# Kernel tuning notes

Measured on AMD Instinct MI355X. Metric: run time of the kernel, lower is better.

Reference implementation:

```python
import jax, jax.numpy as jnp
import numpy as np

N_ENT = 200000; N_USR = 100000; D = 64
E = 1500000; NI = 1000000
HOPS = 2; N_ITER = 3; N_VIRT = 3; N_REL = 11
EPS = 1e-12


def setup_inputs() -> dict:
    key = jax.random.key(0)
    ks = jax.random.split(key, 8)
    entity_emb = jax.random.normal(ks[0], (N_ENT, D), jnp.float32) * 0.1
    user_emb = jax.random.normal(ks[1], (N_USR, D), jnp.float32) * 0.1
    latent_emb = jax.random.normal(ks[2], (N_VIRT, D), jnp.float32)
    rel_weight = jax.random.normal(ks[3], (N_REL - 1, D), jnp.float32)
    # per-hop Aggregator.w, initialized as in the module
    agg_w = jnp.tile(jnp.array([0.4, 0.3, 0.3], jnp.float32), (HOPS, 1))
    edge_index = jax.random.randint(ks[4], (2, E), 0, N_ENT)
    edge_type = jax.random.randint(ks[5], (E,), 1, N_REL)  # values in [1, n_relations-1]
    user_index = jax.random.randint(ks[6], (NI,), 0, N_USR)
    item_index = jax.random.randint(ks[7], (NI,), 0, N_ENT)
    return dict(entity_emb=entity_emb, user_emb=user_emb, latent_emb=latent_emb,
                rel_weight=rel_weight, agg_w=agg_w, edge_index=edge_index,
                edge_type=edge_type, user_index=user_index, item_index=item_index)


def _l2norm(x):
    n = jnp.linalg.norm(x, axis=1, keepdims=True)
    return x / jnp.maximum(n, EPS)


def _squash(u):
    sq = jnp.sum(u * u, axis=1, keepdims=True)  # ||u||^2
    return (sq / (sq + 1.0)) * _l2norm(u)


def _lws_entity(entity_emb, head, tail, mask_f):
    """LWS over a single virtual-relation edge subset (mask_f zeroes other edges).
    Matches torch: neigh is cumulatively sim-scaled across iterations."""
    cnt = jax.ops.segment_sum(mask_f, head, num_segments=N_ENT)
    denom = jnp.maximum(cnt, 1.0)[:, None]
    neigh = entity_emb[tail] * mask_f[:, None]          # [E, D]
    u = None
    for it in range(N_ITER):
        if u is not None:
            sim = jnp.sum(u[head] * neigh, axis=1, keepdims=True)
            neigh = sim * neigh
        u = jax.ops.segment_sum(neigh, head, num_segments=N_ENT) / denom
        if it < N_ITER - 1:
            u = _squash(u)
        u = u + entity_emb
    return u


def _lws_user(entity_emb, user_emb, user_index, item_index):
    """LWS for users; neigh is re-gathered fresh each iteration (as in torch)."""
    ones = jnp.ones((item_index.shape[0],), entity_emb.dtype)
    cnt = jax.ops.segment_sum(ones, user_index, num_segments=N_USR)
    denom = jnp.maximum(cnt, 1.0)[:, None]
    u = None
    for it in range(N_ITER):
        neigh = entity_emb[item_index]                  # [NI, D]
        if u is not None:
            sim = jnp.sum(u[user_index] * neigh, axis=1, keepdims=True)
            neigh = sim * neigh
        u = jax.ops.segment_sum(neigh, user_index, num_segments=N_USR) / denom
        if it < N_ITER - 1:
            u = _squash(u)
        u = u + user_emb
    return u


def reference(entity_emb, user_emb, latent_emb, rel_weight, agg_w,
              edge_index, edge_type, user_index, item_index):
    head, tail = edge_index[0], edge_index[1]
    # relation -> virtual-relation routing (argmax over similarity)
    relation_remap = jnp.argmax(rel_weight @ latent_emb.T, axis=1)   # [n_rel-1]
    et = relation_remap[edge_type - 1]                               # [E] in [0, N_VIRT)

    entity_res = entity_emb
    user_res = user_emb
    ent = entity_emb
    usr = user_emb
    for hop in range(HOPS):
        items = [_lws_entity(ent, head, tail, (et == i).astype(ent.dtype))
                 for i in range(N_VIRT)]
        w = jax.nn.softmax(agg_w[hop])                               # [3]
        entity_agg = w[0] * items[0] + w[1] * items[1] + w[2] * items[2]
        user_agg = _lws_user(ent, usr, user_index, item_index)
        # no dropout (eval mode); normalize + residual
        ent = _l2norm(entity_agg)
        usr = _l2norm(user_agg)
        entity_res = entity_res + ent
        user_res = user_res + usr
    return jnp.concatenate([entity_res, user_res], axis=0)          # [N_ENT+N_USR, D]
```

## Files before the change

### kernel.cpp

```cpp
#include <hip/hip_runtime.h>

#define N_ENT 200000
#define N_USR 100000
#define NT3   700000
#define UKEY0 600000
#define DIM 64
#define NE 1500000
#define NI_ 1000000
#define NTE 2500000
#define NREL1 10
#define NVIRT 3
#define EPSF 1e-12f
#define SCAN_B 1024
#define RE 6
#define RU 12
#define NBUCK 64
#define NPERM (N_ENT + N_USR)
#define NPB   ((NPERM + 255) / 256)

__device__ __forceinline__ float4 f4_zero() { return make_float4(0.f, 0.f, 0.f, 0.f); }
__device__ __forceinline__ float4 f4_add(float4 a, float4 b) {
    return make_float4(a.x + b.x, a.y + b.y, a.z + b.z, a.w + b.w);
}
__device__ __forceinline__ float4 f4_scale(float s, float4 a) {
    return make_float4(s * a.x, s * a.y, s * a.z, s * a.w);
}
__device__ __forceinline__ float4 f4_fma(float s, float4 a, float4 b) {
    return make_float4(fmaf(s, a.x, b.x), fmaf(s, a.y, b.y), fmaf(s, a.z, b.z), fmaf(s, a.w, b.w));
}
__device__ __forceinline__ float f4_dot(float4 a, float4 b) {
    return a.x * b.x + a.y * b.y + a.z * b.z + a.w * b.w;
}

__device__ __forceinline__ float red16(float v) {
    int x;
    x = __builtin_amdgcn_update_dpp(0, __float_as_int(v), 0xB1, 0xF, 0xF, true);
    v += __int_as_float(x);
    x = __builtin_amdgcn_update_dpp(0, __float_as_int(v), 0x4E, 0xF, 0xF, true);
    v += __int_as_float(x);
    x = __builtin_amdgcn_update_dpp(0, __float_as_int(v), 0x124, 0xF, 0xF, true);
    v += __int_as_float(x);
    x = __builtin_amdgcn_update_dpp(0, __float_as_int(v), 0x128, 0xF, 0xF, true);
    v += __int_as_float(x);
    return v;
}

__device__ __forceinline__ float4 squash4(float4 u, float sq) {
    float n = sqrtf(sq);
    float s = sq / ((sq + 1.f) * fmaxf(n, EPSF));
    return f4_scale(s, u);
}

__device__ __forceinline__ void block_remap(const float* __restrict__ rw,
                                            const float* __restrict__ lat,
                                            int* sremap) {
    int t = threadIdx.x;
    if (t < NREL1) {
        float best = -3.4e38f; int bi = 0;
        for (int j = 0; j < NVIRT; j++) {
            float s = 0.f;
            for (int d = 0; d < DIM; d++) s += rw[t * DIM + d] * lat[j * DIM + d];
            if (s > best) { best = s; bi = j; }
        }
        sremap[t] = bi;
    }
    __syncthreads();
}

__global__ void k_count_all(const int* __restrict__ head, const int* __restrict__ etype,
                            const float* __restrict__ rw, const float* __restrict__ lat,
                            const int* __restrict__ uidx, int* __restrict__ cnt) {
    __shared__ int sremap[NREL1];
    block_remap(rw, lat, sremap);
    int i = blockIdx.x * blockDim.x + threadIdx.x;
    if (i < NE) {
        int key = head[i] * 3 + sremap[etype[i] - 1];
        atomicAdd(&cnt[key], 1);
    } else if (i < NTE) {
        atomicAdd(&cnt[UKEY0 + uidx[i - NE]], 1);
    }
}

__global__ void k_scan1(const int* __restrict__ in, int* __restrict__ excl,
                        int* __restrict__ bsum, int n) {
    __shared__ int s[SCAN_B];
    int tid = threadIdx.x, gid = blockIdx.x * SCAN_B + tid;
    int v = (gid < n) ? in[gid] : 0;
    s[tid] = v; __syncthreads();
    for (int off = 1; off < SCAN_B; off <<= 1) {
        int t = 0;
        if (tid >= off) t = s[tid - off];
        __syncthreads();
        s[tid] += t;
        __syncthreads();
    }
    if (gid < n) excl[gid] = s[tid] - v;
    if (tid == SCAN_B - 1) bsum[blockIdx.x] = s[tid];
}

__global__ void k_scan23(const int* __restrict__ excl, const int* __restrict__ bsum,
                         const int* __restrict__ cnt, int* __restrict__ rp,
                         int* __restrict__ cur, int n, int nb) {
    __shared__ int s[SCAN_B];
    int tid = threadIdx.x;
    int v = (tid < nb && tid < (int)blockIdx.x) ? bsum[tid] : 0;
    s[tid] = v;
    __syncthreads();
    for (int off = SCAN_B / 2; off > 0; off >>= 1) {
        if (tid < off) s[tid] += s[tid + off];
        __syncthreads();
    }
    int prefix = s[0];
    int gid = blockIdx.x * SCAN_B + tid;
    if (gid < n) {
        int val = excl[gid] + prefix;
        rp[gid] = val;
        cur[gid] = val;
        if (gid == n - 1) rp[n] = val + cnt[gid];
    }
}

__global__ void k_scatter_all(const int* __restrict__ head, const int* __restrict__ tail,
                              const int* __restrict__ etype,
                              const float* __restrict__ rw, const float* __restrict__ lat,
                              const int* __restrict__ uidx, const int* __restrict__ iidx,
                              int* __restrict__ cur, int* __restrict__ sorted) {
    __shared__ int sremap[NREL1];
    block_remap(rw, lat, sremap);
    int i = blockIdx.x * blockDim.x + threadIdx.x;
    if (i < NE) {
        int key = head[i] * 3 + sremap[etype[i] - 1];
        int pos = atomicAdd(&cur[key], 1);
        sorted[pos] = tail[i];
    } else if (i < NTE) {
        int j = i - NE;
        int pos = atomicAdd(&cur[UKEY0 + uidx[j]], 1);
        sorted[pos] = iidx[j];
    }
}

__device__ __forceinline__ int perm_bucket(const int* __restrict__ rp, int i) {
    if (i < N_ENT) {
        int d = rp[i * 3 + 3] - rp[i * 3];
        return (d < NBUCK) ? d : (NBUCK - 1);
    }
    int u = i - N_ENT;
    int d = rp[UKEY0 + u + 1] - rp[UKEY0 + u];
    return NBUCK + ((d < NBUCK) ? d : (NBUCK - 1));
}

__global__ void k_histL(const int* __restrict__ rp, int* __restrict__ bh) {
    __shared__ int h[2 * NBUCK];
    int t = threadIdx.x;
    if (t < 2 * NBUCK) h[t] = 0;
    __syncthreads();
    int i = blockIdx.x * 256 + t;
    if (i < NPERM) atomicAdd(&h[perm_bucket(rp, i)], 1);
    __syncthreads();
    if (t < 2 * NBUCK) bh[t * NPB + blockIdx.x] = h[t];
}

__global__ void k_histscan(int* __restrict__ bh, int* __restrict__ bt) {
    __shared__ int s[SCAN_B];
    int b = blockIdx.x, t = threadIdx.x;
    int base = b * NPB;
    int i0 = 2 * t, i1 = 2 * t + 1;
    int a0 = (i0 < NPB) ? bh[base + i0] : 0;
    int a1 = (i1 < NPB) ? bh[base + i1] : 0;
    int pair = a0 + a1;
    s[t] = pair; __syncthreads();
    for (int off = 1; off < SCAN_B; off <<= 1) {
        int v = 0;
        if (t >= off) v = s[t - off];
        __syncthreads();
        s[t] += v;
        __syncthreads();
    }
    int exclPair = s[t] - pair;
    if (i0 < NPB) bh[base + i0] = exclPair;
    if (i1 < NPB) bh[base + i1] = exclPair + a0;
    if (t == SCAN_B - 1) bt[b] = s[t];
}

__global__ void k_bucketbase(const int* __restrict__ bt, int* __restrict__ bb) {
    __shared__ int s[2 * NBUCK];
    int t = threadIdx.x;
    int v = bt[t];
    s[t] = v;
    __syncthreads();
    for (int off = 1; off < NBUCK; off <<= 1) {
        int x = 0;
        if (t >= off && ((t - off) >> 6) == (t >> 6)) x = s[t - off];
        __syncthreads();
        s[t] += x;
        __syncthreads();
    }
    bb[t] = s[t] - v;
}

__global__ void k_permb(const int* __restrict__ rp, const int* __restrict__ bh,
                        const int* __restrict__ bb,
                        int* __restrict__ permE, int* __restrict__ permU) {
    __shared__ int cur[2 * NBUCK];
    int t = threadIdx.x;
    if (t < 2 * NBUCK) cur[t] = 0;
    __syncthreads();
    int i = blockIdx.x * 256 + t;
    if (i < NPERM) {
        int b = perm_bucket(rp, i);
        int l = atomicAdd(&cur[b], 1);
        int pos = bb[b] + bh[b * NPB + blockIdx.x] + l;
        if (i < N_ENT) permE[pos] = i;
        else permU[pos] = i - N_ENT;
    }
}

#define NBLK_E (N_ENT / 16)
#define NBLK_U (N_USR / 16)

__global__ __launch_bounds__(256, 5) void k_hop(
    const float* __restrict__ ent, const float* __restrict__ usr,
    const int* __restrict__ rp, const int* __restrict__ sorted,
    const int* __restrict__ permE, const int* __restrict__ permU,
    const float* __restrict__ aw, int hop,
    float* __restrict__ ent_next, float* __restrict__ usr_next,
    int do_store, int first,
    float* __restrict__ outE, float* __restrict__ outU)
{
    int lane = threadIdx.x & 15;
    const float4* entv = (const float4*)ent;

    if (blockIdx.x < NBLK_E) {
        int g = permE[blockIdx.x * 16 + (threadIdx.x >> 4)];
        float4 eh = entv[g * 16 + lane];
        float4 agg = f4_zero();

        float a0 = aw[hop * 3 + 0], a1 = aw[hop * 3 + 1], a2 = aw[hop * 3 + 2];
        float m = fmaxf(a0, fmaxf(a1, a2));
        float e0 = expf(a0 - m), e1 = expf(a1 - m), e2 = expf(a2 - m);
        float esum = e0 + e1 + e2;
        float w0 = e0 / esum, w1 = e1 / esum, w2 = e2 / esum;

        int b3 = g * 3;
        int s0 = rp[b3], s1 = rp[b3 + 1], s2 = rp[b3 + 2], s3 = rp[b3 + 3];
        int dg0 = s1 - s0, dg1 = s2 - s1, dg2 = s3 - s2;
        int myp0 = (lane < dg0) ? sorted[s0 + lane] : 0;
        int myp1 = (lane < dg1) ? sorted[s1 + lane] : 0;
        int myp2 = (lane < dg2) ? sorted[s2 + lane] : 0;

        #pragma unroll
        for (int v = 0; v < NVIRT; v++) {
            int s   = (v == 0) ? s0   : (v == 1) ? s1   : s2;
            int deg = (v == 0) ? dg0  : (v == 1) ? dg1  : dg2;
            int myp = (v == 0) ? myp0 : (v == 1) ? myp1 : myp2;
            float w = (v == 0) ? w0   : (v == 1) ? w1   : w2;
            float inv = 1.f / fmaxf((float)deg, 1.f);

            float4 xc[RE];
            float4 acc = f4_zero();
            #pragma unroll
            for (int r = 0; r < RE; r++) {
                if (r < deg) {
                    int p = __shfl(myp, r, 16);
                    float4 x = entv[p * 16 + lane];
                    xc[r] = x;
                    acc = f4_add(acc, x);
                }
            }
            for (int r = RE; r < deg; r++) {
                int p = (r < 16) ? __shfl(myp, r, 16) : sorted[s + r];
                acc = f4_add(acc, entv[p * 16 + lane]);
            }
            float4 u = f4_scale(inv, acc);
            float sq = red16(f4_dot(u, u));
            float4 u1 = f4_add(squash4(u, sq), eh);

            float4 acc1 = f4_zero();
            float d1c[RE];
            float d1me = 0.f;
            #pragma unroll
            for (int r = 0; r < RE; r++) {
                if (r < deg) {
                    float4 x = xc[r];
                    float d1 = red16(f4_dot(u1, x));
                    d1c[r] = d1;
                    acc1 = f4_fma(d1, x, acc1);
                }
            }
            for (int r = RE; r < deg; r++) {
                int p = (r < 16) ? __shfl(myp, r, 16) : sorted[s + r];
                float4 x = entv[p * 16 + lane];
                float d1 = red16(f4_dot(u1, x));
                if (lane == r) d1me = d1;
                acc1 = f4_fma(d1, x, acc1);
            }
            u = f4_scale(inv, acc1);
            sq = red16(f4_dot(u, u));
            float4 u2 = f4_add(squash4(u, sq), eh);

            float4 acc2 = f4_zero();
            #pragma unroll
            for (int r = 0; r < RE; r++) {
                if (r < deg) {
                    float4 x = xc[r];
                    float d2 = red16(f4_dot(u2, x));
                    float d1 = d1c[r];
                    acc2 = f4_fma(d1 * d1 * d2, x, acc2);
                }
            }
            for (int r = RE; r < deg; r++) {
                int p = (r < 16) ? __shfl(myp, r, 16) : sorted[s + r];
                float4 x = entv[p * 16 + lane];
                float d2 = red16(f4_dot(u2, x));
                float d1 = (r < 16) ? __shfl(d1me, r, 16) : red16(f4_dot(u1, x));
                acc2 = f4_fma(d1 * d1 * d2, x, acc2);
            }
            agg = f4_fma(w * inv, acc2, agg);
        }
        agg = f4_add(agg, eh);
        float sq = red16(f4_dot(agg, agg));
        float nn = sqrtf(sq);
        float4 en = f4_scale(1.f / fmaxf(nn, EPSF), agg);
        if (do_store) ((float4*)ent_next)[g * 16 + lane] = en;
        float4* outv = (float4*)outE;
        float4 base = first ? eh : outv[g * 16 + lane];
        outv[g * 16 + lane] = f4_add(base, en);
    } else {
        int gu = permU[(blockIdx.x - NBLK_E) * 16 + (threadIdx.x >> 4)];
        int s = rp[UKEY0 + gu], e = rp[UKEY0 + gu + 1];
        int deg = e - s;
        const float4* usrv = (const float4*)usr;
        float4 uh = usrv[gu * 16 + lane];
        float inv = 1.f / fmaxf((float)deg, 1.f);

        int deg16 = (deg < 16) ? deg : 16;
        int myp = (lane < deg16) ? sorted[s + lane] : 0;

        float4 xc[RU];
        float4 acc = f4_zero();
        #pragma unroll
        for (int r = 0; r < RU; r++) {
            if (r < deg) {
                int p = __shfl(myp, r, 16);
                float4 x = entv[p * 16 + lane];
                xc[r] = x;
                acc = f4_add(acc, x);
            }
        }
        for (int r = RU; r < deg; r++) {
            int p = (r < 16) ? __shfl(myp, r, 16) : sorted[s + r];
            acc = f4_add(acc, entv[p * 16 + lane]);
        }
        float4 u = f4_scale(inv, acc);
        float sq = red16(f4_dot(u, u));
        float4 u1 = f4_add(squash4(u, sq), uh);

        acc = f4_zero();
        #pragma unroll
        for (int r = 0; r < RU; r++) {
            if (r < deg) {
                float4 x = xc[r];
                acc = f4_fma(red16(f4_dot(u1, x)), x, acc);
            }
        }
        for (int r = RU; r < deg; r++) {
            int p = (r < 16) ? __shfl(myp, r, 16) : sorted[s + r];
            float4 x = entv[p * 16 + lane];
            acc = f4_fma(red16(f4_dot(u1, x)), x, acc);
        }
        u = f4_scale(inv, acc);
        sq = red16(f4_dot(u, u));
        float4 u2 = f4_add(squash4(u, sq), uh);

        acc = f4_zero();
        #pragma unroll
        for (int r = 0; r < RU; r++) {
            if (r < deg) {
                float4 x = xc[r];
                acc = f4_fma(red16(f4_dot(u2, x)), x, acc);
            }
        }
        for (int r = RU; r < deg; r++) {
            int p = (r < 16) ? __shfl(myp, r, 16) : sorted[s + r];
            float4 x = entv[p * 16 + lane];
            acc = f4_fma(red16(f4_dot(u2, x)), x, acc);
        }
        float4 u3 = f4_add(f4_scale(inv, acc), uh);
        sq = red16(f4_dot(u3, u3));
        float nn = sqrtf(sq);
        float4 un = f4_scale(1.f / fmaxf(nn, EPSF), u3);
        if (do_store) ((float4*)usr_next)[gu * 16 + lane] = un;
        float4* outv = (float4*)outU;
        float4 base = first ? uh : outv[gu * 16 + lane];
        outv[gu * 16 + lane] = f4_add(base, un);
    }
}

extern "C" void kernel_launch(void* const* d_in, const int* in_sizes, int n_in,
                              void* d_out, int out_size, void* d_ws, size_t ws_size,
                              hipStream_t stream)
{
    const float* entity_emb = (const float*)d_in[0];
    const float* user_emb   = (const float*)d_in[1];
    const float* latent     = (const float*)d_in[2];
    const float* rel_w      = (const float*)d_in[3];
    const float* agg_w      = (const float*)d_in[4];
    const int* edge_index   = (const int*)d_in[5];
    const int* edge_type    = (const int*)d_in[6];
    const int* user_index   = (const int*)d_in[7];
    const int* item_index   = (const int*)d_in[8];
    float* out = (float*)d_out;

    char* ws = (char*)d_ws;
    size_t off = 0;
    auto alloc = [&](size_t bytes) -> void* {
        void* p = ws + off;
        off += (bytes + 255) / 256 * 256;
        return p;
    };
    float* entA  = (float*)alloc((size_t)N_ENT * DIM * 4);
    float* usrA  = (float*)alloc((size_t)N_USR * DIM * 4);
    int* cnt     = (int*)alloc((size_t)NT3 * 4);
    int* rp      = (int*)alloc((size_t)(NT3 + 1) * 4);
    int* cur     = (int*)alloc((size_t)NT3 * 4);
    int* excl    = (int*)alloc((size_t)NT3 * 4);
    int* bsum    = (int*)alloc(1024 * 4);
    int* sorted  = (int*)alloc((size_t)NTE * 4);
    int* bh      = (int*)alloc((size_t)2 * NBUCK * NPB * 4);
    int* bt      = (int*)alloc(2 * NBUCK * 4);
    int* bb      = (int*)alloc(2 * NBUCK * 4);
    int* permE   = (int*)alloc((size_t)N_ENT * 4);
    int* permU   = (int*)alloc((size_t)N_USR * 4);

    const int* head = edge_index;
    const int* tail = edge_index + NE;

    hipMemsetAsync(cnt, 0, (size_t)NT3 * 4, stream);

    k_count_all<<<(NTE + 255) / 256, 256, 0, stream>>>(
        head, edge_type, rel_w, latent, user_index, cnt);

    int nb = (NT3 + SCAN_B - 1) / SCAN_B;
    k_scan1<<<nb, SCAN_B, 0, stream>>>(cnt, excl, bsum, NT3);
    k_scan23<<<nb, SCAN_B, 0, stream>>>(excl, bsum, cnt, rp, cur, NT3, nb);

    k_scatter_all<<<(NTE + 255) / 256, 256, 0, stream>>>(
        head, tail, edge_type, rel_w, latent, user_index, item_index, cur, sorted);

    k_histL<<<NPB, 256, 0, stream>>>(rp, bh);
    k_histscan<<<2 * NBUCK, SCAN_B, 0, stream>>>(bh, bt);
    k_bucketbase<<<1, 2 * NBUCK, 0, stream>>>(bt, bb);
    k_permb<<<NPB, 256, 0, stream>>>(rp, bh, bb, permE, permU);

    const float* ec = entity_emb;
    const float* uc = user_emb;
    for (int hop = 0; hop < 2; hop++) {
        int do_store = (hop == 0);
        int first = (hop == 0);
        k_hop<<<NBLK_E + NBLK_U, 256, 0, stream>>>(
            ec, uc, rp, sorted, permE, permU, agg_w, hop, entA, usrA, do_store, first,
            out, out + (size_t)N_ENT * DIM);
        ec = entA;
        uc = usrA;
    }
}
```

Measured before the change: 741.3 us.

## Record atomic rank in count pass, drop scatter atomics and bucketbase kernel

The count kernel now stores each edge's atomic return value as its rank, so the scatter pass computes its position as rp[key]+rank with no second atomic and no cursor array. The bucket-base scan is folded into k_permb, which removes one kernel launch. In k_hop the neighbor indices are now read directly from `sorted` inside each loop instead of being preloaded once per lane and broadcast with shuffles. The trade is an extra rank array that is written and then read back, plus more scalar global loads in the hot kernel.

Result: slower. 769.8 us (+3.8%).

```diff
diff --git a/kernel.cpp b/kernel.cpp
--- a/kernel.cpp
+++ b/kernel.cpp
@@ -69,15 +69,16 @@
 
 __global__ void k_count_all(const int* __restrict__ head, const int* __restrict__ etype,
                             const float* __restrict__ rw, const float* __restrict__ lat,
-                            const int* __restrict__ uidx, int* __restrict__ cnt) {
+                            const int* __restrict__ uidx, int* __restrict__ cnt,
+                            int* __restrict__ rank) {
     __shared__ int sremap[NREL1];
     block_remap(rw, lat, sremap);
     int i = blockIdx.x * blockDim.x + threadIdx.x;
     if (i < NE) {
         int key = head[i] * 3 + sremap[etype[i] - 1];
-        atomicAdd(&cnt[key], 1);
+        rank[i] = atomicAdd(&cnt[key], 1);
     } else if (i < NTE) {
-        atomicAdd(&cnt[UKEY0 + uidx[i - NE]], 1);
+        rank[i] = atomicAdd(&cnt[UKEY0 + uidx[i - NE]], 1);
     }
 }
 
@@ -100,7 +101,7 @@
 
 __global__ void k_scan23(const int* __restrict__ excl, const int* __restrict__ bsum,
                          const int* __restrict__ cnt, int* __restrict__ rp,
-                         int* __restrict__ cur, int n, int nb) {
+                         int n, int nb) {
     __shared__ int s[SCAN_B];
     int tid = threadIdx.x;
     int v = (tid < nb && tid < (int)blockIdx.x) ? bsum[tid] : 0;
@@ -115,7 +116,6 @@
     if (gid < n) {
         int val = excl[gid] + prefix;
         rp[gid] = val;
-        cur[gid] = val;
         if (gid == n - 1) rp[n] = val + cnt[gid];
     }
 }
@@ -124,18 +124,17 @@
                               const int* __restrict__ etype,
                               const float* __restrict__ rw, const float* __restrict__ lat,
                               const int* __restrict__ uidx, const int* __restrict__ iidx,
-                              int* __restrict__ cur, int* __restrict__ sorted) {
+                              const int* __restrict__ rp, const int* __restrict__ rank,
+                              int* __restrict__ sorted) {
     __shared__ int sremap[NREL1];
     block_remap(rw, lat, sremap);
     int i = blockIdx.x * blockDim.x + threadIdx.x;
     if (i < NE) {
         int key = head[i] * 3 + sremap[etype[i] - 1];
-        int pos = atomicAdd(&cur[key], 1);
-        sorted[pos] = tail[i];
+        sorted[rp[key] + rank[i]] = tail[i];
     } else if (i < NTE) {
         int j = i - NE;
-        int pos = atomicAdd(&cur[UKEY0 + uidx[j]], 1);
-        sorted[pos] = iidx[j];
+        sorted[rp[UKEY0 + uidx[j]] + rank[i]] = iidx[j];
     }
 }
 
@@ -182,34 +181,29 @@
     if (t == SCAN_B - 1) bt[b] = s[t];
 }
 
-__global__ void k_bucketbase(const int* __restrict__ bt, int* __restrict__ bb) {
-    __shared__ int s[2 * NBUCK];
+__global__ void k_permb(const int* __restrict__ rp, const int* __restrict__ bh,
+                        const int* __restrict__ bt,
+                        int* __restrict__ permE, int* __restrict__ permU) {
+    __shared__ int sb[2 * NBUCK];
+    __shared__ int cur[2 * NBUCK];
     int t = threadIdx.x;
-    int v = bt[t];
-    s[t] = v;
+    int v0 = 0;
+    if (t < 2 * NBUCK) { v0 = bt[t]; sb[t] = v0; cur[t] = 0; }
     __syncthreads();
     for (int off = 1; off < NBUCK; off <<= 1) {
         int x = 0;
-        if (t >= off && ((t - off) >> 6) == (t >> 6)) x = s[t - off];
-        __syncthreads();
-        s[t] += x;
-        __syncthreads();
-    }
-    bb[t] = s[t] - v;
-}
-
-__global__ void k_permb(const int* __restrict__ rp, const int* __restrict__ bh,
-                        const int* __restrict__ bb,
-                        int* __restrict__ permE, int* __restrict__ permU) {
-    __shared__ int cur[2 * NBUCK];
-    int t = threadIdx.x;
-    if (t < 2 * NBUCK) cur[t] = 0;
+        if (t < 2 * NBUCK && t >= off && ((t - off) >> 6) == (t >> 6)) x = sb[t - off];
+        __syncthreads();
+        if (t < 2 * NBUCK) sb[t] += x;
+        __syncthreads();
+    }
+    if (t < 2 * NBUCK) sb[t] -= v0;
     __syncthreads();
     int i = blockIdx.x * 256 + t;
     if (i < NPERM) {
         int b = perm_bucket(rp, i);
         int l = atomicAdd(&cur[b], 1);
-        int pos = bb[b] + bh[b * NPB + blockIdx.x] + l;
+        int pos = sb[b] + bh[b * NPB + blockIdx.x] + l;
         if (i < N_ENT) permE[pos] = i;
         else permU[pos] = i - N_ENT;
     }
@@ -244,15 +238,11 @@
         int b3 = g * 3;
         int s0 = rp[b3], s1 = rp[b3 + 1], s2 = rp[b3 + 2], s3 = rp[b3 + 3];
         int dg0 = s1 - s0, dg1 = s2 - s1, dg2 = s3 - s2;
-        int myp0 = (lane < dg0) ? sorted[s0 + lane] : 0;
-        int myp1 = (lane < dg1) ? sorted[s1 + lane] : 0;
-        int myp2 = (lane < dg2) ? sorted[s2 + lane] : 0;
 
         #pragma unroll
         for (int v = 0; v < NVIRT; v++) {
             int s   = (v == 0) ? s0   : (v == 1) ? s1   : s2;
             int deg = (v == 0) ? dg0  : (v == 1) ? dg1  : dg2;
-            int myp = (v == 0) ? myp0 : (v == 1) ? myp1 : myp2;
             float w = (v == 0) ? w0   : (v == 1) ? w1   : w2;
             float inv = 1.f / fmaxf((float)deg, 1.f);
 
@@ -261,14 +251,14 @@
             #pragma unroll
             for (int r = 0; r < RE; r++) {
                 if (r < deg) {
-                    int p = __shfl(myp, r, 16);
+                    int p = sorted[s + r];
                     float4 x = entv[p * 16 + lane];
                     xc[r] = x;
                     acc = f4_add(acc, x);
                 }
             }
             for (int r = RE; r < deg; r++) {
-                int p = (r < 16) ? __shfl(myp, r, 16) : sorted[s + r];
+                int p = sorted[s + r];
                 acc = f4_add(acc, entv[p * 16 + lane]);
             }
             float4 u = f4_scale(inv, acc);
@@ -288,7 +278,7 @@
                 }
             }
             for (int r = RE; r < deg; r++) {
-                int p = (r < 16) ? __shfl(myp, r, 16) : sorted[s + r];
+                int p = sorted[s + r];
                 float4 x = entv[p * 16 + lane];
                 float d1 = red16(f4_dot(u1, x));
                 if (lane == r) d1me = d1;
@@ -309,7 +299,7 @@
                 }
             }
             for (int r = RE; r < deg; r++) {
-                int p = (r < 16) ? __shfl(myp, r, 16) : sorted[s + r];
+                int p = sorted[s + r];
                 float4 x = entv[p * 16 + lane];
                 float d2 = red16(f4_dot(u2, x));
                 float d1 = (r < 16) ? __shfl(d1me, r, 16) : red16(f4_dot(u1, x));
@@ -333,22 +323,19 @@
         float4 uh = usrv[gu * 16 + lane];
         float inv = 1.f / fmaxf((float)deg, 1.f);
 
-        int deg16 = (deg < 16) ? deg : 16;
-        int myp = (lane < deg16) ? sorted[s + lane] : 0;
-
         float4 xc[RU];
         float4 acc = f4_zero();
         #pragma unroll
         for (int r = 0; r < RU; r++) {
             if (r < deg) {
-                int p = __shfl(myp, r, 16);
+                int p = sorted[s + r];
                 float4 x = entv[p * 16 + lane];
                 xc[r] = x;
                 acc = f4_add(acc, x);
             }
         }
         for (int r = RU; r < deg; r++) {
-            int p = (r < 16) ? __shfl(myp, r, 16) : sorted[s + r];
+            int p = sorted[s + r];
             acc = f4_add(acc, entv[p * 16 + lane]);
         }
         float4 u = f4_scale(inv, acc);
@@ -364,7 +351,7 @@
             }
         }
         for (int r = RU; r < deg; r++) {
-            int p = (r < 16) ? __shfl(myp, r, 16) : sorted[s + r];
+            int p = sorted[s + r];
             float4 x = entv[p * 16 + lane];
             acc = f4_fma(red16(f4_dot(u1, x)), x, acc);
         }
@@ -381,7 +368,7 @@
             }
         }
         for (int r = RU; r < deg; r++) {
-            int p = (r < 16) ? __shfl(myp, r, 16) : sorted[s + r];
+            int p = sorted[s + r];
             float4 x = entv[p * 16 + lane];
             acc = f4_fma(red16(f4_dot(u2, x)), x, acc);
         }
@@ -422,13 +409,12 @@
     float* usrA  = (float*)alloc((size_t)N_USR * DIM * 4);
     int* cnt     = (int*)alloc((size_t)NT3 * 4);
     int* rp      = (int*)alloc((size_t)(NT3 + 1) * 4);
-    int* cur     = (int*)alloc((size_t)NT3 * 4);
     int* excl    = (int*)alloc((size_t)NT3 * 4);
     int* bsum    = (int*)alloc(1024 * 4);
     int* sorted  = (int*)alloc((size_t)NTE * 4);
+    int* rank    = (int*)alloc((size_t)NTE * 4);
     int* bh      = (int*)alloc((size_t)2 * NBUCK * NPB * 4);
     int* bt      = (int*)alloc(2 * NBUCK * 4);
-    int* bb      = (int*)alloc(2 * NBUCK * 4);
     int* permE   = (int*)alloc((size_t)N_ENT * 4);
     int* permU   = (int*)alloc((size_t)N_USR * 4);
 
@@ -438,19 +424,18 @@
     hipMemsetAsync(cnt, 0, (size_t)NT3 * 4, stream);
 
     k_count_all<<<(NTE + 255) / 256, 256, 0, stream>>>(
-        head, edge_type, rel_w, latent, user_index, cnt);
+        head, edge_type, rel_w, latent, user_index, cnt, rank);
 
     int nb = (NT3 + SCAN_B - 1) / SCAN_B;
     k_scan1<<<nb, SCAN_B, 0, stream>>>(cnt, excl, bsum, NT3);
-    k_scan23<<<nb, SCAN_B, 0, stream>>>(excl, bsum, cnt, rp, cur, NT3, nb);
+    k_scan23<<<nb, SCAN_B, 0, stream>>>(excl, bsum, cnt, rp, NT3, nb);
 
     k_scatter_all<<<(NTE + 255) / 256, 256, 0, stream>>>(
-        head, tail, edge_type, rel_w, latent, user_index, item_index, cur, sorted);
+        head, tail, edge_type, rel_w, latent, user_index, item_index, rp, rank, sorted);
 
     k_histL<<<NPB, 256, 0, stream>>>(rp, bh);
     k_histscan<<<2 * NBUCK, SCAN_B, 0, stream>>>(bh, bt);
-    k_bucketbase<<<1, 2 * NBUCK, 0, stream>>>(bt, bb);
-    k_permb<<<NPB, 256, 0, stream>>>(rp, bh, bb, permE, permU);
+    k_permb<<<NPB, 256, 0, stream>>>(rp, bh, bt, permE, permU);
 
     const float* ec = entity_emb;
     const float* uc = user_emb;
```
